# Kernel tuning notes

Measured on AMD Instinct MI355X. Metric: run time of the kernel, lower is better.

The kernel has to match this reference:

```python
import jax, jax.numpy as jnp
import numpy as np

M_TOKENS, D_IN, D_OUT = 4096, 4096, 16384


def setup_inputs() -> dict:
    key = jax.random.key(0)
    k1, k2, k3, k4 = jax.random.split(key, 4)
    x = jax.random.normal(k1, (M_TOKENS, D_IN), dtype=jnp.float32)
    # pre-quantized int8 weight, stored [K, N] as in qweight_kn
    qweight_kn = jax.random.randint(k2, (D_IN, D_OUT), -127, 128, dtype=jnp.int8)
    # per-output-channel weight dequant scales (float16 buffer, used as fp32 in kernel)
    weight_scales = jax.random.uniform(k3, (D_OUT,), dtype=jnp.float32, minval=1e-3, maxval=2e-2)
    bias = jax.random.normal(k4, (D_OUT,), dtype=jnp.float32) * 0.01
    return {"x": x, "qweight_kn": qweight_kn, "weight_scales": weight_scales, "bias": bias}


def reference(x, qweight_kn, weight_scales, bias):
    target_dtype = x.dtype
    x2 = x.reshape(-1, x.shape[-1])  # [M, K]
    # dynamic per-token (per-row) symmetric quantization
    x_max = jnp.max(jnp.abs(x2), axis=-1, keepdims=True).astype(jnp.float32) + 1e-5
    x_scales = x_max / 127.0  # [M, 1]
    x_int8 = jnp.clip(jnp.round(x2.astype(jnp.float32) / x_scales), -128, 127).astype(jnp.int8)
    acc = jax.lax.dot_general(
        x_int8, qweight_kn,
        dimension_numbers=(((1,), (0,)), ((), ())),
        preferred_element_type=jnp.int32,
    )  # [M, N] int32
    # fused dequant: row act-scale * col weight-scale, plus bias
    c = acc.astype(jnp.float32) * x_scales * weight_scales[None, :].astype(jnp.float32)
    c = c + bias[None, :]
    out = c.astype(jnp.bfloat16)  # kernel stores bf16
    return out.reshape(*x.shape[:-1], -1).astype(target_dtype)
```

## Files before the change

### kernel.cpp

```cpp
#include <hip/hip_runtime.h>
#include <hip/hip_bf16.h>
#include <stdint.h>

typedef int v4i __attribute__((ext_vector_type(4)));

#define GM 4096
#define GN 16384
#define GK 4096
#define BM 256
#define BN 256
#define BK 128
#define NTILES (GK / BK)

__device__ __forceinline__ void gload16(const void* g, void* l) {
  __builtin_amdgcn_global_load_lds(
      (const __attribute__((address_space(1))) void*)g,
      (__attribute__((address_space(3))) void*)l, 16, 0, 0);
}

__global__ __launch_bounds__(256) void quant_rows(
    const float* __restrict__ x, int8_t* __restrict__ xq,
    float* __restrict__ xs, int K) {
  const int row = blockIdx.x;
  const int t = threadIdx.x;
  const float4* src = (const float4*)(x + (size_t)row * K) + t * 4;
  float4 v[4];
  float m = 0.f;
#pragma unroll
  for (int i = 0; i < 4; ++i) {
    v[i] = src[i];
    m = fmaxf(m, fmaxf(fmaxf(fabsf(v[i].x), fabsf(v[i].y)),
                       fmaxf(fabsf(v[i].z), fabsf(v[i].w))));
  }
#pragma unroll
  for (int off = 1; off < 64; off <<= 1)
    m = fmaxf(m, __shfl_xor(m, off, 64));
  __shared__ float wmax[4];
  if ((t & 63) == 0) wmax[t >> 6] = m;
  __syncthreads();
  const float gm = fmaxf(fmaxf(wmax[0], wmax[1]), fmaxf(wmax[2], wmax[3]));
  const float scale = (gm + 1e-5f) / 127.0f;
  if (t == 0) xs[row] = scale;
  unsigned packed[4];
#pragma unroll
  for (int i = 0; i < 4; ++i) {
    float fv[4] = {v[i].x, v[i].y, v[i].z, v[i].w};
    unsigned p = 0;
#pragma unroll
    for (int j = 0; j < 4; ++j) {
      int q = (int)rintf(fv[j] / scale);
      q = max(-128, min(127, q));
      p |= (unsigned)(q & 0xff) << (8 * j);
    }
    packed[i] = p;
  }
  *(int4*)(xq + (size_t)row * K + t * 16) =
      make_int4((int)packed[0], (int)packed[1], (int)packed[2], (int)packed[3]);
}

__global__ __launch_bounds__(256) void transpose_pack(
    const int* __restrict__ W32, int8_t* __restrict__ Wt, int K, int N) {
  __shared__ __align__(16) int8_t tile[64][80];
  const int t = threadIdx.x;
  const int n0 = blockIdx.x * 64;
  const int k0 = blockIdx.y * 64;
  const int ln = t & 63;
  const int wv = t >> 6;
#pragma unroll
  for (int it = 0; it < 16; ++it) {
    const int kk = wv * 16 + it;
    tile[ln][kk] = (int8_t)W32[(size_t)(k0 + kk) * N + n0 + ln];
  }
  __syncthreads();
  const int kb = wv * 16;
  const int4 v = *(const int4*)&tile[ln][kb];
  *(int4*)(Wt + (size_t)(n0 + ln) * K + k0 + kb) = v;
}

__global__ __launch_bounds__(512, 2) void gemm_i8(
    const int8_t* __restrict__ Xq, const int8_t* __restrict__ Wt,
    const float* __restrict__ xs, const float* __restrict__ wsc,
    const float* __restrict__ bias, float* __restrict__ C) {
  __shared__ __align__(16) int8_t lA[2][BM][BK];
  __shared__ __align__(16) int8_t lB[2][BN][BK];

  const int t = threadIdx.x;
  const int lane = t & 63;
  const int w = t >> 6;
  const int wr = w >> 2;
  const int wc = w & 3;
  const int fr = lane & 15;
  const int kg = lane >> 4;

  const int bid = blockIdx.x;
  const int xcd = bid & 7;
  const int q = bid >> 3;
  const int tm = q & 15;
  const int tn = xcd * 8 + (q >> 4);
  const size_t rowA0 = (size_t)tm * BM;
  const size_t rowB0 = (size_t)tn * BN;

  const int8_t* XqB = Xq + rowA0 * GK;
  const int8_t* WtB = Wt + rowB0 * GK;
  int srcOff[4], dstOff[4];
#pragma unroll
  for (int i = 0; i < 4; ++i) {
    const int slot0 = (i * 8 + w) * 64;
    const int slot = slot0 + lane;
    const int r = slot >> 3;
    const int c = (slot & 7) ^ (r & 7);
    srcOff[i] = r * GK + c * 16;
    dstOff[i] = slot0 * 16;
  }

#define STAGE(KT, D)                                                        \
  {                                                                         \
    const int ko = (KT)*BK;                                                 \
    _Pragma("unroll") for (int i = 0; i < 4; ++i)                           \
        gload16(XqB + srcOff[i] + ko, (int8_t*)&lA[(D)][0][0] + dstOff[i]); \
    _Pragma("unroll") for (int i = 0; i < 4; ++i)                           \
        gload16(WtB + srcOff[i] + ko, (int8_t*)&lB[(D)][0][0] + dstOff[i]); \
  }

  const int ck0 = ((0 + kg) ^ (fr & 7)) * 16;
  const int ck1 = ((4 + kg) ^ (fr & 7)) * 16;

  v4i acc[8][4] = {};
  v4i areg[4][2], aregh[4][2], breg[4][2];

#define ISSUE_A_LO(D)                                                \
  _Pragma("unroll") for (int mi = 0; mi < 4; ++mi) {                 \
    const int8_t* p = &lA[(D)][wr * 128 + mi * 16 + fr][0];          \
    areg[mi][0] = *(const v4i*)(p + ck0);                            \
    areg[mi][1] = *(const v4i*)(p + ck1);                            \
  }
#define ISSUE_A_HI(D)                                                \
  _Pragma("unroll") for (int mi = 0; mi < 4; ++mi) {                 \
    const int8_t* p = &lA[(D)][wr * 128 + 64 + mi * 16 + fr][0];     \
    aregh[mi][0] = *(const v4i*)(p + ck0);                           \
    aregh[mi][1] = *(const v4i*)(p + ck1);                           \
  }
#define ISSUE_B(NJ, D)                                               \
  {                                                                  \
    const int8_t* p = &lB[(D)][wc * 64 + (NJ)*16 + fr][0];           \
    breg[NJ][0] = *(const v4i*)(p + ck0);                            \
    breg[NJ][1] = *(const v4i*)(p + ck1);                            \
  }

#define MFMA_Q(AR, MI0, NJ0)                                                    \
  _Pragma("unroll") for (int mi = 0; mi < 4; ++mi)                              \
      _Pragma("unroll") for (int nj = 0; nj < 2; ++nj) {                        \
    acc[(MI0) + mi][(NJ0) + nj] = __builtin_amdgcn_mfma_i32_16x16x64_i8(        \
        AR[mi][0], breg[(NJ0) + nj][0], acc[(MI0) + mi][(NJ0) + nj], 0, 0, 0);  \
    acc[(MI0) + mi][(NJ0) + nj] = __builtin_amdgcn_mfma_i32_16x16x64_i8(        \
        AR[mi][1], breg[(NJ0) + nj][1], acc[(MI0) + mi][(NJ0) + nj], 0, 0, 0);  \
  }

  STAGE(0, 0);
  STAGE(1, 1);
  asm volatile("s_waitcnt vmcnt(8)" ::: "memory");
  __builtin_amdgcn_s_barrier();
  ISSUE_A_LO(0);

  for (int kt = 0; kt < NTILES; ++kt) {
    const int d = kt & 1;
    ISSUE_B(0, d);
    ISSUE_B(1, d);
    ISSUE_B(2, d);
    ISSUE_B(3, d);
    ISSUE_A_HI(d);
    asm volatile("s_waitcnt lgkmcnt(12)" ::: "memory");
    __builtin_amdgcn_sched_barrier(0);
    __builtin_amdgcn_s_setprio(1);
    MFMA_Q(areg, 0, 0);
    __builtin_amdgcn_s_setprio(0);
    asm volatile("s_waitcnt lgkmcnt(8)" ::: "memory");
    __builtin_amdgcn_sched_barrier(0);
    __builtin_amdgcn_s_setprio(1);
    MFMA_Q(areg, 0, 2);
    __builtin_amdgcn_s_setprio(0);
    asm volatile("s_waitcnt lgkmcnt(0)" ::: "memory");
    __builtin_amdgcn_sched_barrier(0);
    __builtin_amdgcn_s_barrier();
    if (kt + 2 < NTILES) {
      STAGE(kt + 2, d);
      asm volatile("s_waitcnt vmcnt(8)" ::: "memory");
    } else {
      asm volatile("s_waitcnt vmcnt(0)" ::: "memory");
    }
    __builtin_amdgcn_s_barrier();
    if (kt + 1 < NTILES) { ISSUE_A_LO(d ^ 1); }
    __builtin_amdgcn_sched_barrier(0);
    __builtin_amdgcn_s_setprio(1);
    MFMA_Q(aregh, 4, 0);
    MFMA_Q(aregh, 4, 2);
    __builtin_amdgcn_s_setprio(0);
  }

  float xsv[8][4];
#pragma unroll
  for (int mi = 0; mi < 8; ++mi)
#pragma unroll
    for (int r = 0; r < 4; ++r)
      xsv[mi][r] = xs[rowA0 + wr * 128 + mi * 16 + kg * 4 + r];
#pragma unroll
  for (int nj = 0; nj < 4; ++nj) {
    const int col_l = wc * 64 + nj * 16 + fr;
    const float wsv = wsc[rowB0 + col_l];
    const float bv = bias[rowB0 + col_l];
#pragma unroll
    for (int mi = 0; mi < 8; ++mi) {
#pragma unroll
      for (int r = 0; r < 4; ++r) {
        const size_t row = rowA0 + wr * 128 + mi * 16 + kg * 4 + r;
        const float f = (float)acc[mi][nj][r] * xsv[mi][r] * wsv + bv;
        C[row * GN + rowB0 + col_l] = __bfloat162float(__float2bfloat16(f));
      }
    }
  }
}

extern "C" void kernel_launch(void* const* d_in, const int* in_sizes, int n_in,
                              void* d_out, int out_size, void* d_ws, size_t ws_size,
                              hipStream_t stream) {
  const int M = GM, K = GK, N = GN;
  const float* x = (const float*)d_in[0];
  const int* W32 = (const int*)d_in[1];
  const float* wsc = (const float*)d_in[2];
  const float* bias = (const float*)d_in[3];
  float* out = (float*)d_out;

  float* xs = (float*)d_ws;
  int8_t* Xq = (int8_t*)d_ws + 16384;
  int8_t* Wt = (int8_t*)d_ws + 16384 + (size_t)M * K;

  transpose_pack<<<dim3(N / 64, K / 64), 256, 0, stream>>>(W32, Wt, K, N);
  quant_rows<<<M, 256, 0, stream>>>(x, Xq, xs, K);
  gemm_i8<<<dim3((M / BM) * (N / BN)), 512, 0, stream>>>(Xq, Wt, xs, wsc, bias,
                                                         out);
}
```

Measured before the change: 506.9 us.

## Switch GEMM to 32x32x32 int8 MFMA and simplify the double-buffer pipeline

Replaces the 16x16x64 int8 MFMA tiling with 32x32x32 MFMA tiles, so each wave holds 4x2 16-wide accumulators and reads A/B fragments with four k-slices per row. The main loop now waits for each stage, then issues the next stage's global-to-LDS load up front, instead of the earlier prefetch-two-ahead scheme with a split lo/hi A register set. The larger MFMA shape is meant to cut LDS read traffic per FLOP and improve matrix-core efficiency. The cost is that only one stage is in flight, and the wait of vmcnt(0) at the top of each iteration can expose global load latency. The epilogue reads scales directly per row.

```diff
diff --git a/kernel.cpp b/kernel.cpp
--- a/kernel.cpp
+++ b/kernel.cpp
@@ -3,6 +3,7 @@
 #include <stdint.h>
 
 typedef int v4i __attribute__((ext_vector_type(4)));
+typedef int v16i __attribute__((ext_vector_type(16)));
 
 #define GM 4096
 #define GN 16384
@@ -89,8 +90,8 @@
   const int w = t >> 6;
   const int wr = w >> 2;
   const int wc = w & 3;
-  const int fr = lane & 15;
-  const int kg = lane >> 4;
+  const int l31 = lane & 31;
+  const int kg2 = lane >> 5;
 
   const int bid = blockIdx.x;
   const int xcd = bid & 7;
@@ -122,98 +123,81 @@
         gload16(WtB + srcOff[i] + ko, (int8_t*)&lB[(D)][0][0] + dstOff[i]); \
   }
 
-  const int ck0 = ((0 + kg) ^ (fr & 7)) * 16;
-  const int ck1 = ((4 + kg) ^ (fr & 7)) * 16;
-
-  v4i acc[8][4] = {};
-  v4i areg[4][2], aregh[4][2], breg[4][2];
-
-#define ISSUE_A_LO(D)                                                \
-  _Pragma("unroll") for (int mi = 0; mi < 4; ++mi) {                 \
-    const int8_t* p = &lA[(D)][wr * 128 + mi * 16 + fr][0];          \
-    areg[mi][0] = *(const v4i*)(p + ck0);                            \
-    areg[mi][1] = *(const v4i*)(p + ck1);                            \
-  }
-#define ISSUE_A_HI(D)                                                \
-  _Pragma("unroll") for (int mi = 0; mi < 4; ++mi) {                 \
-    const int8_t* p = &lA[(D)][wr * 128 + 64 + mi * 16 + fr][0];     \
-    aregh[mi][0] = *(const v4i*)(p + ck0);                           \
-    aregh[mi][1] = *(const v4i*)(p + ck1);                           \
-  }
-#define ISSUE_B(NJ, D)                                               \
-  {                                                                  \
-    const int8_t* p = &lB[(D)][wc * 64 + (NJ)*16 + fr][0];           \
-    breg[NJ][0] = *(const v4i*)(p + ck0);                            \
-    breg[NJ][1] = *(const v4i*)(p + ck1);                            \
-  }
-
-#define MFMA_Q(AR, MI0, NJ0)                                                    \
-  _Pragma("unroll") for (int mi = 0; mi < 4; ++mi)                              \
-      _Pragma("unroll") for (int nj = 0; nj < 2; ++nj) {                        \
-    acc[(MI0) + mi][(NJ0) + nj] = __builtin_amdgcn_mfma_i32_16x16x64_i8(        \
-        AR[mi][0], breg[(NJ0) + nj][0], acc[(MI0) + mi][(NJ0) + nj], 0, 0, 0);  \
-    acc[(MI0) + mi][(NJ0) + nj] = __builtin_amdgcn_mfma_i32_16x16x64_i8(        \
-        AR[mi][1], breg[(NJ0) + nj][1], acc[(MI0) + mi][(NJ0) + nj], 0, 0, 0);  \
-  }
+  int ck[4];
+#pragma unroll
+  for (int s = 0; s < 4; ++s) ck[s] = ((2 * s + kg2) ^ (l31 & 7)) * 16;
+
+  v16i acc[4][2] = {};
+  v4i areg[4][4], breg[2][4];
+
+#define RD_A(MI, D)                                                 \
+  {                                                                 \
+    const int8_t* p = &lA[(D)][wr * 128 + (MI)*32 + l31][0];        \
+    _Pragma("unroll") for (int s = 0; s < 4; ++s)                   \
+        areg[MI][s] = *(const v4i*)(p + ck[s]);                     \
+  }
+#define RD_B(NJ, D)                                                 \
+  {                                                                 \
+    const int8_t* p = &lB[(D)][wc * 64 + (NJ)*32 + l31][0];         \
+    _Pragma("unroll") for (int s = 0; s < 4; ++s)                   \
+        breg[NJ][s] = *(const v4i*)(p + ck[s]);                     \
+  }
+
+#define MFMA_F(MI, NJ)                                                        \
+  _Pragma("unroll") for (int s = 0; s < 4; ++s)                               \
+      acc[MI][NJ] = __builtin_amdgcn_mfma_i32_32x32x32_i8(                    \
+          areg[MI][s], breg[NJ][s], acc[MI][NJ], 0, 0, 0);
 
   STAGE(0, 0);
-  STAGE(1, 1);
-  asm volatile("s_waitcnt vmcnt(8)" ::: "memory");
-  __builtin_amdgcn_s_barrier();
-  ISSUE_A_LO(0);
 
   for (int kt = 0; kt < NTILES; ++kt) {
     const int d = kt & 1;
-    ISSUE_B(0, d);
-    ISSUE_B(1, d);
-    ISSUE_B(2, d);
-    ISSUE_B(3, d);
-    ISSUE_A_HI(d);
+    asm volatile("s_waitcnt vmcnt(0)" ::: "memory");
+    __builtin_amdgcn_s_barrier();
+    if (kt + 1 < NTILES) STAGE(kt + 1, d ^ 1);
+    RD_A(0, d);
+    RD_A(1, d);
+    RD_B(0, d);
+    __builtin_amdgcn_sched_barrier(0);
+    RD_B(1, d);
+    __builtin_amdgcn_sched_barrier(0);
+    RD_A(2, d);
+    RD_A(3, d);
+    __builtin_amdgcn_sched_barrier(0);
     asm volatile("s_waitcnt lgkmcnt(12)" ::: "memory");
     __builtin_amdgcn_sched_barrier(0);
     __builtin_amdgcn_s_setprio(1);
-    MFMA_Q(areg, 0, 0);
+    MFMA_F(0, 0);
+    MFMA_F(1, 0);
     __builtin_amdgcn_s_setprio(0);
     asm volatile("s_waitcnt lgkmcnt(8)" ::: "memory");
     __builtin_amdgcn_sched_barrier(0);
     __builtin_amdgcn_s_setprio(1);
-    MFMA_Q(areg, 0, 2);
+    MFMA_F(0, 1);
+    MFMA_F(1, 1);
     __builtin_amdgcn_s_setprio(0);
     asm volatile("s_waitcnt lgkmcnt(0)" ::: "memory");
     __builtin_amdgcn_sched_barrier(0);
-    __builtin_amdgcn_s_barrier();
-    if (kt + 2 < NTILES) {
-      STAGE(kt + 2, d);
-      asm volatile("s_waitcnt vmcnt(8)" ::: "memory");
-    } else {
-      asm volatile("s_waitcnt vmcnt(0)" ::: "memory");
-    }
-    __builtin_amdgcn_s_barrier();
-    if (kt + 1 < NTILES) { ISSUE_A_LO(d ^ 1); }
-    __builtin_amdgcn_sched_barrier(0);
     __builtin_amdgcn_s_setprio(1);
-    MFMA_Q(aregh, 4, 0);
-    MFMA_Q(aregh, 4, 2);
+    MFMA_F(2, 0);
+    MFMA_F(3, 0);
+    MFMA_F(2, 1);
+    MFMA_F(3, 1);
     __builtin_amdgcn_s_setprio(0);
   }
 
-  float xsv[8][4];
-#pragma unroll
-  for (int mi = 0; mi < 8; ++mi)
-#pragma unroll
-    for (int r = 0; r < 4; ++r)
-      xsv[mi][r] = xs[rowA0 + wr * 128 + mi * 16 + kg * 4 + r];
-#pragma unroll
-  for (int nj = 0; nj < 4; ++nj) {
-    const int col_l = wc * 64 + nj * 16 + fr;
+#pragma unroll
+  for (int nj = 0; nj < 2; ++nj) {
+    const int col_l = wc * 64 + nj * 32 + l31;
     const float wsv = wsc[rowB0 + col_l];
     const float bv = bias[rowB0 + col_l];
 #pragma unroll
-    for (int mi = 0; mi < 8; ++mi) {
-#pragma unroll
-      for (int r = 0; r < 4; ++r) {
-        const size_t row = rowA0 + wr * 128 + mi * 16 + kg * 4 + r;
-        const float f = (float)acc[mi][nj][r] * xsv[mi][r] * wsv + bv;
+    for (int mi = 0; mi < 4; ++mi) {
+#pragma unroll
+      for (int r = 0; r < 16; ++r) {
+        const size_t row =
+            rowA0 + wr * 128 + mi * 32 + (r & 3) + 8 * (r >> 2) + 4 * kg2;
+        const float f = (float)acc[mi][nj][r] * xs[row] * wsv + bv;
         C[row * GN + rowB0 + col_l] = __bfloat162float(__float2bfloat16(f));
       }
     }
```

Result: faster. 486.7 us (-4.0%).
